# Performance work log

Measured on AMD Instinct MI355X. Metric: run time of the kernel, lower is better.

Reference implementation:

```python
import jax, jax.numpy as jnp
import numpy as np

TEMPERATURE = 0.5
EPS_NORM = 1e-12   # F.normalize eps
EPS_DEN = 1e-8     # denominator clamp


def setup_inputs() -> dict:
    key = jax.random.key(0)
    k1, k2 = jax.random.split(key)
    B, D = 4096, 256
    return {
        "proj_feat1": jax.random.normal(k1, (B, D), dtype=jnp.float32),
        "proj_feat2": jax.random.normal(k2, (B, D), dtype=jnp.float32),
    }


def _l2_normalize(x):
    n = jnp.sqrt(jnp.sum(x * x, axis=1, keepdims=True))
    return x / jnp.maximum(n, EPS_NORM)


def reference(proj_feat1, proj_feat2):
    B = proj_feat1.shape[0]
    z1 = _l2_normalize(proj_feat1)
    z2 = _l2_normalize(proj_feat2)
    z = jnp.concatenate([z1, z2], axis=0)          # [2B, D], unit rows
    # cosine similarity of unit-norm rows == plain matmul (GEMM instead of
    # the O(N^2*D) broadcasted intermediate in the torch source)
    sim = jnp.matmul(z, z.T)                        # [2B, 2B]
    s = jnp.exp(sim / TEMPERATURE)                  # [2B, 2B]
    idx = jnp.arange(2 * B)
    pos_idx = (idx + B) % (2 * B)                   # roll(eye, B, dim=1) positions
    numerator = s[idx, pos_idx]                     # [2B]
    # negatives: everything except the diagonal
    diag = jnp.diagonal(s)
    denominator = jnp.sum(s, axis=1) - diag         # sum * (1 - eye)
    denominator = jnp.maximum(denominator, EPS_DEN)
    loss = jnp.mean(-jnp.log(numerator / denominator))
    return loss
```

## Files before the change

kernel.cpp:

```cpp
#include <hip/hip_runtime.h>
#include <hip/hip_bf16.h>

#define NTOT 8192
#define BB   4096
#define DD   256
#define NBLK 512
#define NSTEPS 2112

typedef __attribute__((ext_vector_type(8))) short short8v;
typedef __attribute__((ext_vector_type(4))) float f32x4;

__device__ __forceinline__ unsigned short f2bf(float f) {
    union { __hip_bfloat16 h; unsigned short u; } cv;
    cv.h = __float2bfloat16(f);
    return cv.u;
}

__global__ __launch_bounds__(256) void k_normalize(
    const float* __restrict__ x1, const float* __restrict__ x2,
    unsigned short* __restrict__ zbf,
    float* __restrict__ selfdot, float* __restrict__ posdot,
    float* __restrict__ S, float* __restrict__ out)
{
    if (blockIdx.x < 8) {
        float4 z4 = make_float4(0.f, 0.f, 0.f, 0.f);
        *(float4*)(S + blockIdx.x * 1024 + threadIdx.x * 4) = z4;
        if (blockIdx.x == 0 && threadIdx.x == 0) out[0] = 0.0f;
    }

    const int lane = threadIdx.x & 63;
    const int pair = blockIdx.x * 4 + (threadIdx.x >> 6);

    const float4 a = *(const float4*)(x1 + (size_t)pair * DD + lane * 4);
    const float4 b = *(const float4*)(x2 + (size_t)pair * DD + lane * 4);

    float s1 = a.x * a.x + a.y * a.y + a.z * a.z + a.w * a.w;
    float s2 = b.x * b.x + b.y * b.y + b.z * b.z + b.w * b.w;
#pragma unroll
    for (int off = 1; off < 64; off <<= 1) {
        s1 += __shfl_xor(s1, off);
        s2 += __shfl_xor(s2, off);
    }
    const float inv1 = 1.0f / fmaxf(sqrtf(s1), 1e-12f);
    const float inv2 = 1.0f / fmaxf(sqrtf(s2), 1e-12f);

    const float4 z1 = make_float4(a.x * inv1, a.y * inv1, a.z * inv1, a.w * inv1);
    const float4 z2 = make_float4(b.x * inv2, b.y * inv2, b.z * inv2, b.w * inv2);

    float sd1 = z1.x * z1.x + z1.y * z1.y + z1.z * z1.z + z1.w * z1.w;
    float sd2 = z2.x * z2.x + z2.y * z2.y + z2.z * z2.z + z2.w * z2.w;
    float pd  = z1.x * z2.x + z1.y * z2.y + z1.z * z2.z + z1.w * z2.w;
#pragma unroll
    for (int off = 1; off < 64; off <<= 1) {
        sd1 += __shfl_xor(sd1, off);
        sd2 += __shfl_xor(sd2, off);
        pd  += __shfl_xor(pd, off);
    }

    ushort4 u1, u2;
    u1.x = f2bf(z1.x); u1.y = f2bf(z1.y); u1.z = f2bf(z1.z); u1.w = f2bf(z1.w);
    u2.x = f2bf(z2.x); u2.y = f2bf(z2.y); u2.z = f2bf(z2.z); u2.w = f2bf(z2.w);
    *(ushort4*)(zbf + (size_t)pair * DD + lane * 4) = u1;
    *(ushort4*)(zbf + (size_t)(pair + BB) * DD + lane * 4) = u2;

    if (lane == 0) {
        selfdot[pair] = sd1;
        selfdot[pair + BB] = sd2;
        posdot[pair] = pd;
        posdot[pair + BB] = pd;
    }
}

__global__ __launch_bounds__(256, 2) void k_simsum(
    const unsigned short* __restrict__ zbf, float* __restrict__ S)
{
    __shared__ char Bsh[2][32768];

    const int tid  = threadIdx.x;
    const int lane = tid & 63;
    const int wave = tid >> 6;
    const int frow = lane & 15;

    const int b = blockIdx.x;
    const int sBeg = (33 * b) >> 3;
    const int sEnd = (33 * (b + 1)) >> 3;

    int ai = 0;
    {
        int C = 0;
        while (C + 128 - 4 * ai <= sBeg) { C += 128 - 4 * ai; ++ai; }
    }
    int C2 = 0;
    for (int k = 0; k < ai; ++k) C2 += 128 - 4 * k;
    int ct = sBeg - C2;

    const int jswz = (tid & 31) ^ ((tid >> 5) & 7);
    const int stageOff = (tid >> 5) * 512 + jswz * 16;

    const int base0 = frow * 512 + (lane >> 4) * 16;
    const int bmask = (frow & 7) << 4;
    int addrs[8];
#pragma unroll
    for (int kk = 0; kk < 8; ++kk) addrs[kk] = (base0 + kk * 64) ^ bmask;

    short8v Afrag[4][8];
#pragma unroll
    for (int rt = 0; rt < 4; ++rt) {
        const unsigned short* ap =
            zbf + (size_t)(256 * ai + wave * 64 + rt * 16 + frow) * DD + (lane >> 4) * 8;
#pragma unroll
        for (int kk = 0; kk < 8; ++kk)
            Afrag[rt][kk] = *(const short8v*)(ap + kk * 32);
    }

    float rs[4][4];
#pragma unroll
    for (int rt = 0; rt < 4; ++rt)
#pragma unroll
        for (int q = 0; q < 4; ++q) rs[rt][q] = 0.0f;

#define COLBASE(ii, tt) ((tt) < 4 ? 256 * (ii) + 64 * (tt) : 256 * ((ii) + 1) + 64 * ((tt) - 4))

#define STAGE(cb, bufidx)                                                          \
    do {                                                                           \
        const char* gs_ = (const char*)zbf + (size_t)(cb) * 512 + stageOff;        \
        char* ld_ = &Bsh[bufidx][0] + tid * 16;                                    \
        _Pragma("unroll")                                                          \
        for (int r_ = 0; r_ < 8; ++r_)                                             \
            __builtin_amdgcn_global_load_lds(                                      \
                (const __attribute__((address_space(1))) unsigned int*)(gs_ + r_ * 4096), \
                (__attribute__((address_space(3))) unsigned int*)(ld_ + r_ * 4096),\
                16, 0, 0);                                                         \
    } while (0)

    STAGE(COLBASE(ai, ct), 0);
    __syncthreads();

    int cur = 0;
    int ci = ai, cstep = ct;
    for (int s = sBeg; s < sEnd; ++s) {
        int ni = ci, nt = cstep + 1;
        if (nt >= 128 - 4 * ci) { ni = ci + 1; nt = 0; }
        if (s + 1 < sEnd) STAGE(COLBASE(ni, nt), cur ^ 1);

        const int  colbase = COLBASE(ci, cstep);
        const bool isUpper = (cstep >= 4);
        const char* bsh = &Bsh[cur][0];

#pragma unroll
        for (int c2 = 0; c2 < 2; ++c2) {
            const char* bc = bsh + c2 * 16384;
            f32x4 acc[4][2];
#pragma unroll
            for (int rt = 0; rt < 4; ++rt)
#pragma unroll
                for (int c = 0; c < 2; ++c) {
                    acc[rt][c][0] = 0.0f; acc[rt][c][1] = 0.0f;
                    acc[rt][c][2] = 0.0f; acc[rt][c][3] = 0.0f;
                }

#pragma unroll
            for (int kk = 0; kk < 8; ++kk) {
                const short8v b0 = *(const short8v*)(bc + addrs[kk]);
                const short8v b1 = *(const short8v*)(bc + addrs[kk] + 8192);
#pragma unroll
                for (int rt = 0; rt < 4; ++rt) {
                    acc[rt][0] = __builtin_amdgcn_mfma_f32_16x16x32_bf16(
                        Afrag[rt][kk], b0, acc[rt][0], 0, 0, 0);
                    acc[rt][1] = __builtin_amdgcn_mfma_f32_16x16x32_bf16(
                        Afrag[rt][kk], b1, acc[rt][1], 0, 0, 0);
                }
            }

            float cs0 = 0.0f, cs1 = 0.0f;
#pragma unroll
            for (int rt = 0; rt < 4; ++rt)
#pragma unroll
                for (int q = 0; q < 4; ++q) {
                    const float e0 = exp2f(acc[rt][0][q] * 2.8853900817779268f);
                    const float e1 = exp2f(acc[rt][1][q] * 2.8853900817779268f);
                    rs[rt][q] += e0 + e1;
                    cs0 += e0; cs1 += e1;
                }
            if (isUpper) {
                cs0 += __shfl_xor(cs0, 16); cs0 += __shfl_xor(cs0, 32);
                cs1 += __shfl_xor(cs1, 16); cs1 += __shfl_xor(cs1, 32);
                if (lane < 16) {
                    atomicAdd(&S[colbase + c2 * 32 + frow], cs0);
                    atomicAdd(&S[colbase + c2 * 32 + 16 + frow], cs1);
                }
            }
        }

        if (s + 1 < sEnd && ni != ai) {
#pragma unroll
            for (int rt = 0; rt < 4; ++rt)
#pragma unroll
                for (int q = 0; q < 4; ++q) {
                    float v = rs[rt][q];
                    v += __shfl_xor(v, 1);
                    v += __shfl_xor(v, 2);
                    v += __shfl_xor(v, 4);
                    v += __shfl_xor(v, 8);
                    if (frow == 0)
                        atomicAdd(&S[256 * ai + wave * 64 + rt * 16 + (lane >> 4) * 4 + q], v);
                    rs[rt][q] = 0.0f;
                }
            ai = ni;
#pragma unroll
            for (int rt = 0; rt < 4; ++rt) {
                const unsigned short* ap =
                    zbf + (size_t)(256 * ai + wave * 64 + rt * 16 + frow) * DD + (lane >> 4) * 8;
#pragma unroll
                for (int kk = 0; kk < 8; ++kk)
                    Afrag[rt][kk] = *(const short8v*)(ap + kk * 32);
            }
        }
        ci = ni; cstep = nt;

        __syncthreads();
        cur ^= 1;
    }

#pragma unroll
    for (int rt = 0; rt < 4; ++rt)
#pragma unroll
        for (int q = 0; q < 4; ++q) {
            float v = rs[rt][q];
            v += __shfl_xor(v, 1);
            v += __shfl_xor(v, 2);
            v += __shfl_xor(v, 4);
            v += __shfl_xor(v, 8);
            if (frow == 0)
                atomicAdd(&S[256 * ai + wave * 64 + rt * 16 + (lane >> 4) * 4 + q], v);
        }
#undef STAGE
#undef COLBASE
}

__global__ __launch_bounds__(256) void k_final(
    const float* __restrict__ S, const float* __restrict__ selfdot,
    const float* __restrict__ posdot, float* __restrict__ out)
{
    __shared__ float red[4];
    const int tid = threadIdx.x;
    const int i = blockIdx.x * 256 + tid;
    const float den = fmaxf(S[i] - expf(2.0f * selfdot[i]), 1e-8f);
    float acc = logf(den) - 2.0f * posdot[i];
#pragma unroll
    for (int off = 1; off < 64; off <<= 1) acc += __shfl_xor(acc, off);
    if ((tid & 63) == 0) red[tid >> 6] = acc;
    __syncthreads();
    if (tid == 0)
        atomicAdd(out, (red[0] + red[1] + red[2] + red[3]) * (1.0f / (float)NTOT));
}

extern "C" void kernel_launch(void* const* d_in, const int* in_sizes, int n_in,
                              void* d_out, int out_size, void* d_ws, size_t ws_size,
                              hipStream_t stream) {
    const float* x1 = (const float*)d_in[0];
    const float* x2 = (const float*)d_in[1];
    float* out = (float*)d_out;

    char* ws = (char*)d_ws;
    unsigned short* zbf = (unsigned short*)ws;
    size_t off = (size_t)NTOT * DD * sizeof(unsigned short);
    float* S = (float*)(ws + off);
    off += (size_t)NTOT * sizeof(float);
    float* selfdot = (float*)(ws + off);
    off += (size_t)NTOT * sizeof(float);
    float* posdot = (float*)(ws + off);

    k_normalize<<<dim3(BB / 4), dim3(256), 0, stream>>>(x1, x2, zbf, selfdot, posdot, S, out);
    k_simsum<<<dim3(NBLK), dim3(256), 0, stream>>>(zbf, S);
    k_final<<<dim3(NTOT / 256), dim3(256), 0, stream>>>(S, selfdot, posdot, out);
}
```

Baseline: 100.6 us.

## Decouple waves in similarity GEMM with per-wave LDS double buffering

```diff
diff --git a/kernel.cpp b/kernel.cpp
--- a/kernel.cpp
+++ b/kernel.cpp
@@ -4,8 +4,9 @@
 #define NTOT 8192
 #define BB   4096
 #define DD   256
-#define NBLK 512
-#define NSTEPS 2112
+#define NWAVES 2048
+#define NBLK (NWAVES / 4)
+#define NCHUNK 33024
 
 typedef __attribute__((ext_vector_type(8))) short short8v;
 typedef __attribute__((ext_vector_type(4))) float f32x4;
@@ -74,40 +75,58 @@
 __global__ __launch_bounds__(256, 2) void k_simsum(
     const unsigned short* __restrict__ zbf, float* __restrict__ S)
 {
-    __shared__ char Bsh[2][32768];
+    __shared__ char Bsh[4][2][8192];
 
     const int tid  = threadIdx.x;
     const int lane = tid & 63;
-    const int wave = tid >> 6;
+    const int wv   = tid >> 6;
     const int frow = lane & 15;
-
-    const int b = blockIdx.x;
-    const int sBeg = (33 * b) >> 3;
-    const int sEnd = (33 * (b + 1)) >> 3;
-
-    int ai = 0;
-    {
-        int C = 0;
-        while (C + 128 - 4 * ai <= sBeg) { C += 128 - 4 * ai; ++ai; }
-    }
-    int C2 = 0;
-    for (int k = 0; k < ai; ++k) C2 += 128 - 4 * k;
-    int ct = sBeg - C2;
-
-    const int jswz = (tid & 31) ^ ((tid >> 5) & 7);
-    const int stageOff = (tid >> 5) * 512 + jswz * 16;
-
-    const int base0 = frow * 512 + (lane >> 4) * 16;
+    const int g    = lane >> 4;
+    const int v    = blockIdx.x * 4 + wv;
+
+    const int sBeg = (129 * v) >> 3;
+    const int sEnd = (129 * (v + 1)) >> 3;
+
+    int r = 0, C = 0;
+    while (C + 512 - 4 * r <= sBeg) { C += 512 - 4 * r; ++r; }
+    int t = sBeg - C;
+
+    int srcOff[8];
+#pragma unroll
+    for (int ri = 0; ri < 8; ++ri) {
+        const int lc = ri * 2 + (lane >> 5);
+        srcOff[ri] = lc * 512 + (((lane & 31) ^ (lc & 7)) << 4);
+    }
+
+    const int base0 = frow * 512 + g * 16;
     const int bmask = (frow & 7) << 4;
     int addrs[8];
 #pragma unroll
     for (int kk = 0; kk < 8; ++kk) addrs[kk] = (base0 + kk * 64) ^ bmask;
 
+    char* buf0 = &Bsh[wv][0][0];
+    char* buf1 = &Bsh[wv][1][0];
+
+#define STAGE(r_, t_, bufp)                                                        \
+    do {                                                                           \
+        const char* gs_ = (const char*)zbf + (size_t)(r_) * 32768                  \
+                          + (size_t)(t_) * 8192;                                   \
+        _Pragma("unroll")                                                          \
+        for (int ri_ = 0; ri_ < 8; ++ri_)                                          \
+            __builtin_amdgcn_global_load_lds(                                      \
+                (const __attribute__((address_space(1))) unsigned int*)(gs_ + srcOff[ri_]), \
+                (__attribute__((address_space(3))) unsigned int*)((bufp) + ri_ * 1024 + lane * 16), \
+                16, 0, 0);                                                         \
+    } while (0)
+
+#define ADV(rr, tt)                                                                \
+    do { if (++(tt) >= 512 - 4 * (rr)) { ++(rr); (tt) = 0; } } while (0)
+
     short8v Afrag[4][8];
 #pragma unroll
     for (int rt = 0; rt < 4; ++rt) {
         const unsigned short* ap =
-            zbf + (size_t)(256 * ai + wave * 64 + rt * 16 + frow) * DD + (lane >> 4) * 8;
+            zbf + (size_t)(64 * r + rt * 16 + frow) * DD + g * 8;
 #pragma unroll
         for (int kk = 0; kk < 8; ++kk)
             Afrag[rt][kk] = *(const short8v*)(ap + kk * 32);
@@ -119,106 +138,85 @@
 #pragma unroll
         for (int q = 0; q < 4; ++q) rs[rt][q] = 0.0f;
 
-#define COLBASE(ii, tt) ((tt) < 4 ? 256 * (ii) + 64 * (tt) : 256 * ((ii) + 1) + 64 * ((tt) - 4))
-
-#define STAGE(cb, bufidx)                                                          \
-    do {                                                                           \
-        const char* gs_ = (const char*)zbf + (size_t)(cb) * 512 + stageOff;        \
-        char* ld_ = &Bsh[bufidx][0] + tid * 16;                                    \
-        _Pragma("unroll")                                                          \
-        for (int r_ = 0; r_ < 8; ++r_)                                             \
-            __builtin_amdgcn_global_load_lds(                                      \
-                (const __attribute__((address_space(1))) unsigned int*)(gs_ + r_ * 4096), \
-                (__attribute__((address_space(3))) unsigned int*)(ld_ + r_ * 4096),\
-                16, 0, 0);                                                         \
-    } while (0)
-
-    STAGE(COLBASE(ai, ct), 0);
-    __syncthreads();
+    STAGE(r, t, buf0);
+    int pr = r, pt = t;
+    ADV(pr, pt);
+    STAGE(pr, pt, buf1);
+    ADV(pr, pt);
 
     int cur = 0;
-    int ci = ai, cstep = ct;
+    int cr = r, ct = t;
     for (int s = sBeg; s < sEnd; ++s) {
-        int ni = ci, nt = cstep + 1;
-        if (nt >= 128 - 4 * ci) { ni = ci + 1; nt = 0; }
-        if (s + 1 < sEnd) STAGE(COLBASE(ni, nt), cur ^ 1);
-
-        const int  colbase = COLBASE(ci, cstep);
-        const bool isUpper = (cstep >= 4);
-        const char* bsh = &Bsh[cur][0];
-
-#pragma unroll
-        for (int c2 = 0; c2 < 2; ++c2) {
-            const char* bc = bsh + c2 * 16384;
-            f32x4 acc[4][2];
+        if (s + 1 < sEnd) {
+            asm volatile("s_waitcnt vmcnt(8)" ::: "memory");
+        } else {
+            asm volatile("s_waitcnt vmcnt(0)" ::: "memory");
+        }
+        __builtin_amdgcn_sched_barrier(0);
+
+        char* buf = cur ? buf1 : buf0;
+
+        f32x4 acc[4];
+#pragma unroll
+        for (int rt = 0; rt < 4; ++rt) {
+            acc[rt][0] = 0.0f; acc[rt][1] = 0.0f;
+            acc[rt][2] = 0.0f; acc[rt][3] = 0.0f;
+        }
+#pragma unroll
+        for (int kk = 0; kk < 8; ++kk) {
+            const short8v bfr = *(const short8v*)(buf + addrs[kk]);
 #pragma unroll
             for (int rt = 0; rt < 4; ++rt)
-#pragma unroll
-                for (int c = 0; c < 2; ++c) {
-                    acc[rt][c][0] = 0.0f; acc[rt][c][1] = 0.0f;
-                    acc[rt][c][2] = 0.0f; acc[rt][c][3] = 0.0f;
-                }
-
-#pragma unroll
-            for (int kk = 0; kk < 8; ++kk) {
-                const short8v b0 = *(const short8v*)(bc + addrs[kk]);
-                const short8v b1 = *(const short8v*)(bc + addrs[kk] + 8192);
+                acc[rt] = __builtin_amdgcn_mfma_f32_16x16x32_bf16(
+                    Afrag[rt][kk], bfr, acc[rt], 0, 0, 0);
+        }
+
+        float cs = 0.0f;
+#pragma unroll
+        for (int rt = 0; rt < 4; ++rt)
+#pragma unroll
+            for (int q = 0; q < 4; ++q) {
+                const float e = exp2f(acc[rt][q] * 2.8853900817779268f);
+                rs[rt][q] += e;
+                cs += e;
+            }
+        if (ct >= 4) {
+            cs += __shfl_xor(cs, 16);
+            cs += __shfl_xor(cs, 32);
+            if (lane < 16)
+                atomicAdd(&S[64 * cr + 16 * ct + frow], cs);
+        }
+
+        if (s + 2 < sEnd) { STAGE(pr, pt, buf); ADV(pr, pt); }
+
+        if (s + 1 < sEnd) {
+            int nr = cr, nt = ct + 1;
+            if (nt >= 512 - 4 * cr) { nr = cr + 1; nt = 0; }
+            if (nr != cr) {
+#pragma unroll
+                for (int rt = 0; rt < 4; ++rt)
+#pragma unroll
+                    for (int q = 0; q < 4; ++q) {
+                        float val = rs[rt][q];
+                        val += __shfl_xor(val, 1);
+                        val += __shfl_xor(val, 2);
+                        val += __shfl_xor(val, 4);
+                        val += __shfl_xor(val, 8);
+                        if (frow == 0)
+                            atomicAdd(&S[64 * cr + rt * 16 + g * 4 + q], val);
+                        rs[rt][q] = 0.0f;
+                    }
 #pragma unroll
                 for (int rt = 0; rt < 4; ++rt) {
-                    acc[rt][0] = __builtin_amdgcn_mfma_f32_16x16x32_bf16(
-                        Afrag[rt][kk], b0, acc[rt][0], 0, 0, 0);
-                    acc[rt][1] = __builtin_amdgcn_mfma_f32_16x16x32_bf16(
-                        Afrag[rt][kk], b1, acc[rt][1], 0, 0, 0);
+                    const unsigned short* ap =
+                        zbf + (size_t)(64 * nr + rt * 16 + frow) * DD + g * 8;
+#pragma unroll
+                    for (int kk = 0; kk < 8; ++kk)
+                        Afrag[rt][kk] = *(const short8v*)(ap + kk * 32);
                 }
             }
-
-            float cs0 = 0.0f, cs1 = 0.0f;
-#pragma unroll
-            for (int rt = 0; rt < 4; ++rt)
-#pragma unroll
-                for (int q = 0; q < 4; ++q) {
-                    const float e0 = exp2f(acc[rt][0][q] * 2.8853900817779268f);
-                    const float e1 = exp2f(acc[rt][1][q] * 2.8853900817779268f);
-                    rs[rt][q] += e0 + e1;
-                    cs0 += e0; cs1 += e1;
-                }
-            if (isUpper) {
-                cs0 += __shfl_xor(cs0, 16); cs0 += __shfl_xor(cs0, 32);
-                cs1 += __shfl_xor(cs1, 16); cs1 += __shfl_xor(cs1, 32);
-                if (lane < 16) {
-                    atomicAdd(&S[colbase + c2 * 32 + frow], cs0);
-                    atomicAdd(&S[colbase + c2 * 32 + 16 + frow], cs1);
-                }
-            }
-        }
-
-        if (s + 1 < sEnd && ni != ai) {
-#pragma unroll
-            for (int rt = 0; rt < 4; ++rt)
-#pragma unroll
-                for (int q = 0; q < 4; ++q) {
-                    float v = rs[rt][q];
-                    v += __shfl_xor(v, 1);
-                    v += __shfl_xor(v, 2);
-                    v += __shfl_xor(v, 4);
-                    v += __shfl_xor(v, 8);
-                    if (frow == 0)
-                        atomicAdd(&S[256 * ai + wave * 64 + rt * 16 + (lane >> 4) * 4 + q], v);
-                    rs[rt][q] = 0.0f;
-                }
-            ai = ni;
-#pragma unroll
-            for (int rt = 0; rt < 4; ++rt) {
-                const unsigned short* ap =
-                    zbf + (size_t)(256 * ai + wave * 64 + rt * 16 + frow) * DD + (lane >> 4) * 8;
-#pragma unroll
-                for (int kk = 0; kk < 8; ++kk)
-                    Afrag[rt][kk] = *(const short8v*)(ap + kk * 32);
-            }
-        }
-        ci = ni; cstep = nt;
-
-        __syncthreads();
+            cr = nr; ct = nt;
+        }
         cur ^= 1;
     }
 
@@ -226,16 +224,16 @@
     for (int rt = 0; rt < 4; ++rt)
 #pragma unroll
         for (int q = 0; q < 4; ++q) {
-            float v = rs[rt][q];
-            v += __shfl_xor(v, 1);
-            v += __shfl_xor(v, 2);
-            v += __shfl_xor(v, 4);
-            v += __shfl_xor(v, 8);
+            float val = rs[rt][q];
+            val += __shfl_xor(val, 1);
+            val += __shfl_xor(val, 2);
+            val += __shfl_xor(val, 4);
+            val += __shfl_xor(val, 8);
             if (frow == 0)
-                atomicAdd(&S[256 * ai + wave * 64 + rt * 16 + (lane >> 4) * 4 + q], v);
+                atomicAdd(&S[64 * cr + rt * 16 + g * 4 + q], val);
         }
 #undef STAGE
-#undef COLBASE
+#undef ADV
 }
 
 __global__ __launch_bounds__(256) void k_final(
```

After: 104.6 us. +4.0%, slower.
